# Kernel tuning notes

Hardware: AMD Instinct MI355X
Metric: run time of the kernel (lower is better)

Reference implementation:

```python
import jax, jax.numpy as jnp
import numpy as np

N = 16777216  # length of the returns series


def setup_inputs() -> dict:
    key = jax.random.key(0)
    returns = 0.01 * jax.random.normal(key, (N,), dtype=jnp.float32)
    return {
        "returns": returns,
        "omega": jnp.float32(0.01),
        "alpha": jnp.float32(0.1),
        "beta": jnp.float32(0.85),
    }


def reference(returns, omega, alpha, beta):
    # GARCH(1,1): h[0] = var(returns) (unbiased, matching torch.var default);
    # h[t] = omega + alpha * r[t-1]^2 + beta * h[t-1]
    h0 = jnp.var(returns, ddof=1)
    # drivers b_t = omega + alpha * r_{t-1}^2 for t = 1..n-1
    b = omega + alpha * jnp.square(returns[:-1])

    def step(h_prev, b_t):
        h_t = b_t + beta * h_prev
        return h_t, h_t

    _, h_rest = jax.lax.scan(step, h0, b)
    h = jnp.concatenate([h0[None], h_rest])  # [n]
    return jnp.sqrt(h), h
```

## Files before the change

### kernel.cpp

```cpp
#include <hip/hip_runtime.h>
#include <math.h>


#define KPW 2048
#define MAIN_BLOCK 256
#define FIXN 160

__global__ __launch_bounds__(MAIN_BLOCK, 8)
void garch_main(const float* __restrict__ r, int n,
                const float* __restrict__ pOmega, const float* __restrict__ pAlpha,
                const float* __restrict__ pBeta,
                double* __restrict__ partial,
                float* __restrict__ out_sqrt, float* __restrict__ out_h) {
    const int lane = threadIdx.x & 63;
    const int wid  = threadIdx.x >> 6;
    const int gwave = blockIdx.x * (MAIN_BLOCK >> 6) + wid;
    const int start = gwave * KPW;

    const float omega = *pOmega;
    const float alpha = *pAlpha;
    const float beta  = *pBeta;

    double s_acc = 0.0, q_acc = 0.0;

    if (start < n) {
        const float c1 = beta;
        const float c2 = c1 * c1;
        const float c3 = c2 * c1;
        const float c4 = c2 * c2;
        const float c8 = c4 * c4;
        const float c16 = c8 * c8;
        const float c32 = c16 * c16;
        const float c64 = c32 * c32;

        float pw1 = 1.0f;
        {
            float p = beta; int e = lane;
            if (e & 1)  pw1 *= p; p *= p;
            if (e & 2)  pw1 *= p; p *= p;
            if (e & 4)  pw1 *= p; p *= p;
            if (e & 8)  pw1 *= p; p *= p;
            if (e & 16) pw1 *= p; p *= p;
            if (e & 32) pw1 *= p;
        }
        float pw4 = 1.0f;
        {
            float p = c4; int e = lane;
            if (e & 1)  pw4 *= p; p *= p;
            if (e & 2)  pw4 *= p; p *= p;
            if (e & 4)  pw4 *= p; p *= p;
            if (e & 8)  pw4 *= p; p *= p;
            if (e & 16) pw4 *= p; p *= p;
            if (e & 32) pw4 *= p;
        }

        float h_prev, r_carry;
        if (start == 0) {
            h_prev = 0.0f;
            r_carry = 0.0f;
        } else {
            float ra = r[start - 2 - lane];
            float ba = fmaf(alpha * ra, ra, omega);
            float part = pw1 * ba;
            for (int d = 1; d < 64; d <<= 1) part += __shfl_xor(part, d, 64);
            h_prev = part;
            r_carry = r[start - 1];
        }

        int end = start + KPW; if (end > n) end = n;
        const float4* r4p = (const float4*)r;
        const int idx0 = (start >> 2) + lane;
        const int iters = (end - start) >> 8;

        float4 rv;
        if (iters > 0) rv = r4p[idx0];
        for (int it = 0; it < iters; ++it) {
            float4 nx;
            if (it + 1 < iters) nx = r4p[idx0 + ((it + 1) << 6)];

            float sp = (rv.x + rv.y) + (rv.z + rv.w);
            float qp = (rv.x * rv.x + rv.y * rv.y)
                     + (rv.z * rv.z + rv.w * rv.w);
            s_acc += (double)sp;
            q_acc += (double)qp;

            float prev = __shfl_up(rv.w, 1, 64);
            if (lane == 0) prev = r_carry;

            float b0 = fmaf(alpha * prev, prev, omega);
            float b1 = fmaf(alpha * rv.x, rv.x, omega);
            float b2 = fmaf(alpha * rv.y, rv.y, omega);
            float b3 = fmaf(alpha * rv.z, rv.z, omega);

            float B = fmaf(c1, b2, b3);
            B = fmaf(c2, b1, B);
            B = fmaf(c3, b0, B);

            float t;
            t = __shfl_up(B, 1, 64);  if (lane >= 1)  B = fmaf(c4,  t, B);
            t = __shfl_up(B, 2, 64);  if (lane >= 2)  B = fmaf(c8,  t, B);
            t = __shfl_up(B, 4, 64);  if (lane >= 4)  B = fmaf(c16, t, B);
            t = __shfl_up(B, 8, 64);  if (lane >= 8)  B = fmaf(c32, t, B);
            t = __shfl_up(B, 16, 64); if (lane >= 16) B = fmaf(c64, t, B);

            float Bex = __shfl_up(B, 1, 64);
            if (lane == 0) Bex = 0.0f;
            float h_base = fmaf(pw4, h_prev, Bex);

            float h0v = fmaf(c1, h_base, b0);
            float h1v = fmaf(c1, h0v, b1);
            float h2v = fmaf(c1, h1v, b2);
            float h3v = fmaf(c1, h2v, b3);

            const int s = start + (it << 8);
            int idx4 = (s >> 2) + lane;
            reinterpret_cast<float4*>(out_sqrt)[idx4] =
                make_float4(sqrtf(h0v), sqrtf(h1v), sqrtf(h2v), sqrtf(h3v));
            reinterpret_cast<float4*>(out_h)[idx4] =
                make_float4(h0v, h1v, h2v, h3v);

            h_prev  = __shfl(h3v, 63, 64);
            r_carry = __shfl(rv.w, 63, 64);
            rv = nx;
        }

        int s = start + (iters << 8);
        if (s < end && lane == 0) {
            float h = h_prev;
            for (int tt = s; tt < end; ++tt) {
                float rr = (tt > 0) ? r[tt - 1] : 0.0f;
                double dv = (double)rr;
                s_acc += dv; q_acc += dv * dv;
                float b = fmaf(alpha * rr, rr, omega);
                float hv = fmaf(beta, h, b);
                out_sqrt[tt] = sqrtf(hv);
                out_h[tt] = hv;
                h = hv;
            }
        }
    }

    for (int d = 1; d < 64; d <<= 1) {
        s_acc += __shfl_xor(s_acc, d, 64);
        q_acc += __shfl_xor(q_acc, d, 64);
    }
    __shared__ double ls[MAIN_BLOCK / 64], lq[MAIN_BLOCK / 64];
    if (lane == 0) { ls[wid] = s_acc; lq[wid] = q_acc; }
    __syncthreads();
    if (threadIdx.x == 0) {
        double S = 0.0, Q = 0.0;
        for (int w = 0; w < MAIN_BLOCK / 64; ++w) { S += ls[w]; Q += lq[w]; }
        partial[2 * blockIdx.x]     = S;
        partial[2 * blockIdx.x + 1] = Q;
    }
}

__global__ __launch_bounds__(256)
void garch_fixup(const float* __restrict__ r, int n,
                 const double* __restrict__ partial, int nparts,
                 const float* __restrict__ pOmega, const float* __restrict__ pAlpha,
                 const float* __restrict__ pBeta,
                 float* __restrict__ out_sqrt, float* __restrict__ out_h) {
    double s = 0.0, q = 0.0;
    for (int i = threadIdx.x; i < nparts; i += blockDim.x) {
        s += partial[2 * i];
        q += partial[2 * i + 1];
    }
    for (int d = 1; d < 64; d <<= 1) {
        s += __shfl_xor(s, d, 64);
        q += __shfl_xor(q, d, 64);
    }
    __shared__ double ls[4], lq[4];
    int wid = threadIdx.x >> 6, lane = threadIdx.x & 63;
    if (lane == 0) { ls[wid] = s; lq[wid] = q; }

    __shared__ float rs[FIXN];
    int m = (FIXN < n) ? FIXN : n;
    if (threadIdx.x < m) rs[threadIdx.x] = r[threadIdx.x];
    __syncthreads();

    if (threadIdx.x == 0) {
        double S = 0.0, Q = 0.0;
        for (int w = 0; w < 4; ++w) { S += ls[w]; Q += lq[w]; }
        double mean = S / (double)n;
        double var = (Q - (double)n * mean * mean) / (double)(n - 1);
        const float omega = *pOmega;
        const float alpha = *pAlpha;
        const float beta  = *pBeta;
        float h = (float)var;
        out_h[0] = h;
        out_sqrt[0] = sqrtf(h);
        for (int t = 1; t < m; ++t) {
            float rr = rs[t - 1];
            float b = fmaf(alpha * rr, rr, omega);
            h = fmaf(beta, h, b);
            out_h[t] = h;
            out_sqrt[t] = sqrtf(h);
        }
    }
}

extern "C" void kernel_launch(void* const* d_in, const int* in_sizes, int n_in,
                              void* d_out, int out_size, void* d_ws, size_t ws_size,
                              hipStream_t stream) {
    const float* r      = (const float*)d_in[0];
    const float* pOmega = (const float*)d_in[1];
    const float* pAlpha = (const float*)d_in[2];
    const float* pBeta  = (const float*)d_in[3];
    int n = in_sizes[0];

    float* out_sqrt = (float*)d_out;
    float* out_h    = out_sqrt + n;

    double* partial = (double*)d_ws;

    const int elems_per_block = KPW * (MAIN_BLOCK / 64);
    const int nblocks = (n + elems_per_block - 1) / elems_per_block;

    garch_main<<<nblocks, MAIN_BLOCK, 0, stream>>>(
        r, n, pOmega, pAlpha, pBeta, partial, out_sqrt, out_h);
    garch_fixup<<<1, 256, 0, stream>>>(
        r, n, partial, nblocks, pOmega, pAlpha, pBeta, out_sqrt, out_h);
}
```

Measured before the change: 202.7 us.

## Restructure scan to 16 elements per lane via LDS transpose

Each wave now handles batches of 1024 elements. Coalesced float4 loads are transposed through padded LDS so each lane holds 16 consecutive returns and runs a serial 16-step local recurrence. This shrinks the cross-lane shuffle scan from five steps to two per batch, and results are transposed back through LDS for coalesced stores. It trades shuffle latency for LDS traffic and more registers, and launch bounds drop occupancy from 8 to 4 blocks.

```diff
diff --git a/kernel.cpp b/kernel.cpp
--- a/kernel.cpp
+++ b/kernel.cpp
@@ -2,20 +2,25 @@
 #include <math.h>
 
 
-#define KPW 2048
+#define K 16
+#define ROWLEN 20
+#define BATCH 1024
+#define NB 2
 #define MAIN_BLOCK 256
+#define WPB (MAIN_BLOCK/64)
 #define FIXN 160
 
-__global__ __launch_bounds__(MAIN_BLOCK, 8)
+__global__ __launch_bounds__(MAIN_BLOCK, 4)
 void garch_main(const float* __restrict__ r, int n,
                 const float* __restrict__ pOmega, const float* __restrict__ pAlpha,
                 const float* __restrict__ pBeta,
                 double* __restrict__ partial,
                 float* __restrict__ out_sqrt, float* __restrict__ out_h) {
+    __shared__ float lds[WPB][64 * ROWLEN];
     const int lane = threadIdx.x & 63;
     const int wid  = threadIdx.x >> 6;
-    const int gwave = blockIdx.x * (MAIN_BLOCK >> 6) + wid;
-    const int start = gwave * KPW;
+    const int gwave = blockIdx.x * WPB + wid;
+    const int wstart = gwave * (BATCH * NB);
 
     const float omega = *pOmega;
     const float alpha = *pAlpha;
@@ -23,10 +28,8 @@
 
     double s_acc = 0.0, q_acc = 0.0;
 
-    if (start < n) {
-        const float c1 = beta;
-        const float c2 = c1 * c1;
-        const float c3 = c2 * c1;
+    if (wstart < n) {
+        const float c2 = beta * beta;
         const float c4 = c2 * c2;
         const float c8 = c4 * c4;
         const float c16 = c8 * c8;
@@ -43,99 +46,102 @@
             if (e & 16) pw1 *= p; p *= p;
             if (e & 32) pw1 *= p;
         }
-        float pw4 = 1.0f;
-        {
-            float p = c4; int e = lane;
-            if (e & 1)  pw4 *= p; p *= p;
-            if (e & 2)  pw4 *= p; p *= p;
-            if (e & 4)  pw4 *= p; p *= p;
-            if (e & 8)  pw4 *= p; p *= p;
-            if (e & 16) pw4 *= p; p *= p;
-            if (e & 32) pw4 *= p;
-        }
-
-        float h_prev, r_carry;
-        if (start == 0) {
-            h_prev = 0.0f;
-            r_carry = 0.0f;
-        } else {
-            float ra = r[start - 2 - lane];
+        float pw16l;
+        { float a2 = pw1 * pw1; float a4 = a2 * a2; float a8 = a4 * a4; pw16l = a8 * a8; }
+
+        float Wp = 0.0f, rm1 = 0.0f;
+        if (wstart > 0) {
+            float ra = r[wstart - 2 - lane];
             float ba = fmaf(alpha * ra, ra, omega);
             float part = pw1 * ba;
             for (int d = 1; d < 64; d <<= 1) part += __shfl_xor(part, d, 64);
-            h_prev = part;
-            r_carry = r[start - 1];
-        }
-
-        int end = start + KPW; if (end > n) end = n;
+            Wp = part;
+            rm1 = r[wstart - 1];
+        }
+
+        float* buf = &lds[wid][0];
         const float4* r4p = (const float4*)r;
-        const int idx0 = (start >> 2) + lane;
-        const int iters = (end - start) >> 8;
-
-        float4 rv;
-        if (iters > 0) rv = r4p[idx0];
-        for (int it = 0; it < iters; ++it) {
-            float4 nx;
-            if (it + 1 < iters) nx = r4p[idx0 + ((it + 1) << 6)];
-
-            float sp = (rv.x + rv.y) + (rv.z + rv.w);
-            float qp = (rv.x * rv.x + rv.y * rv.y)
-                     + (rv.z * rv.z + rv.w * rv.w);
-            s_acc += (double)sp;
-            q_acc += (double)qp;
-
-            float prev = __shfl_up(rv.w, 1, 64);
-            if (lane == 0) prev = r_carry;
-
-            float b0 = fmaf(alpha * prev, prev, omega);
-            float b1 = fmaf(alpha * rv.x, rv.x, omega);
-            float b2 = fmaf(alpha * rv.y, rv.y, omega);
-            float b3 = fmaf(alpha * rv.z, rv.z, omega);
-
-            float B = fmaf(c1, b2, b3);
-            B = fmaf(c2, b1, B);
-            B = fmaf(c3, b0, B);
-
-            float t;
-            t = __shfl_up(B, 1, 64);  if (lane >= 1)  B = fmaf(c4,  t, B);
-            t = __shfl_up(B, 2, 64);  if (lane >= 2)  B = fmaf(c8,  t, B);
-            t = __shfl_up(B, 4, 64);  if (lane >= 4)  B = fmaf(c16, t, B);
-            t = __shfl_up(B, 8, 64);  if (lane >= 8)  B = fmaf(c32, t, B);
-            t = __shfl_up(B, 16, 64); if (lane >= 16) B = fmaf(c64, t, B);
-
-            float Bex = __shfl_up(B, 1, 64);
-            if (lane == 0) Bex = 0.0f;
-            float h_base = fmaf(pw4, h_prev, Bex);
-
-            float h0v = fmaf(c1, h_base, b0);
-            float h1v = fmaf(c1, h0v, b1);
-            float h2v = fmaf(c1, h1v, b2);
-            float h3v = fmaf(c1, h2v, b3);
-
-            const int s = start + (it << 8);
-            int idx4 = (s >> 2) + lane;
-            reinterpret_cast<float4*>(out_sqrt)[idx4] =
-                make_float4(sqrtf(h0v), sqrtf(h1v), sqrtf(h2v), sqrtf(h3v));
-            reinterpret_cast<float4*>(out_h)[idx4] =
-                make_float4(h0v, h1v, h2v, h3v);
-
-            h_prev  = __shfl(h3v, 63, 64);
-            r_carry = __shfl(rv.w, 63, 64);
-            rv = nx;
-        }
-
-        int s = start + (iters << 8);
-        if (s < end && lane == 0) {
-            float h = h_prev;
-            for (int tt = s; tt < end; ++tt) {
-                float rr = (tt > 0) ? r[tt - 1] : 0.0f;
-                double dv = (double)rr;
-                s_acc += dv; q_acc += dv * dv;
-                float b = fmaf(alpha * rr, rr, omega);
-                float hv = fmaf(beta, h, b);
-                out_sqrt[tt] = sqrtf(hv);
-                out_h[tt] = hv;
-                h = hv;
+        float4* oh4 = (float4*)out_h;
+        float4* os4 = (float4*)out_sqrt;
+
+        for (int bi = 0; bi < NB; ++bi) {
+            const int base = wstart + bi * BATCH;
+            if (base >= n) break;
+            if (base + BATCH <= n) {
+                float sp = 0.0f, qp = 0.0f;
+                #pragma unroll
+                for (int j = 0; j < 4; ++j) {
+                    float4 v = r4p[(base >> 2) + (j << 6) + lane];
+                    sp += (v.x + v.y) + (v.z + v.w);
+                    qp += (v.x * v.x + v.y * v.y) + (v.z * v.z + v.w * v.w);
+                    int row = (j << 4) + (lane >> 2);
+                    *(float4*)&buf[row * ROWLEN + 4 * (lane & 3)] = v;
+                }
+                s_acc += (double)sp; q_acc += (double)qp;
+
+                float rl[K];
+                #pragma unroll
+                for (int m = 0; m < 4; ++m) {
+                    float4 v = *(float4*)&buf[lane * ROWLEN + 4 * m];
+                    rl[4*m+0] = v.x; rl[4*m+1] = v.y; rl[4*m+2] = v.z; rl[4*m+3] = v.w;
+                }
+                float pr = __shfl_up(rl[K-1], 1, 64);
+                if (lane == 0) pr = rm1;
+
+                float bl[K];
+                float W = 0.0f;
+                float prv = pr;
+                #pragma unroll
+                for (int k = 0; k < K; ++k) {
+                    float b = fmaf(alpha * prv, prv, omega);
+                    bl[k] = b;
+                    W = fmaf(beta, W, b);
+                    prv = rl[k];
+                }
+
+                float t1 = __shfl_up(W, 1, 64);
+                float Y1 = (lane >= 1) ? fmaf(c16, t1, W) : W;
+                float t2 = __shfl_up(Y1, 2, 64);
+                float Y2 = (lane >= 2) ? fmaf(c32, t2, Y1) : Y1;
+                float sd = __shfl_up(Y2, 1, 64);
+                if (lane == 0) sd = 0.0f;
+                float seed = fmaf(pw16l, Wp, sd);
+
+                float Wtop  = __shfl(Y2, 63, 64);
+                float rlast = __shfl(rl[K-1], 63, 64);
+
+                float h = seed;
+                #pragma unroll
+                for (int m = 0; m < 4; ++m) {
+                    float h0 = fmaf(beta, h,  bl[4*m+0]);
+                    float h1 = fmaf(beta, h0, bl[4*m+1]);
+                    float h2 = fmaf(beta, h1, bl[4*m+2]);
+                    float h3 = fmaf(beta, h2, bl[4*m+3]);
+                    *(float4*)&buf[lane * ROWLEN + 4 * m] = make_float4(h0, h1, h2, h3);
+                    h = h3;
+                }
+
+                #pragma unroll
+                for (int j = 0; j < 4; ++j) {
+                    int row = (j << 4) + (lane >> 2);
+                    float4 hv = *(float4*)&buf[row * ROWLEN + 4 * (lane & 3)];
+                    int idx4 = (base >> 2) + (j << 6) + lane;
+                    oh4[idx4] = hv;
+                    os4[idx4] = make_float4(sqrtf(hv.x), sqrtf(hv.y),
+                                            sqrtf(hv.z), sqrtf(hv.w));
+                }
+
+                Wp  = fmaf(c64, Wp, Wtop);
+                rm1 = rlast;
+            } else if (lane == 0) {
+                float h = Wp;
+                for (int tt = base; tt < n; ++tt) {
+                    float rr = (tt > 0) ? r[tt - 1] : 0.0f;
+                    double dv = (double)rr; s_acc += dv; q_acc += dv * dv;
+                    float b = fmaf(alpha * rr, rr, omega);
+                    h = fmaf(beta, h, b);
+                    out_h[tt] = h; out_sqrt[tt] = sqrtf(h);
+                }
             }
         }
     }
@@ -144,12 +150,12 @@
         s_acc += __shfl_xor(s_acc, d, 64);
         q_acc += __shfl_xor(q_acc, d, 64);
     }
-    __shared__ double ls[MAIN_BLOCK / 64], lq[MAIN_BLOCK / 64];
-    if (lane == 0) { ls[wid] = s_acc; lq[wid] = q_acc; }
+    __shared__ double lsum[WPB], lsq[WPB];
+    if (lane == 0) { lsum[wid] = s_acc; lsq[wid] = q_acc; }
     __syncthreads();
     if (threadIdx.x == 0) {
         double S = 0.0, Q = 0.0;
-        for (int w = 0; w < MAIN_BLOCK / 64; ++w) { S += ls[w]; Q += lq[w]; }
+        for (int w = 0; w < WPB; ++w) { S += lsum[w]; Q += lsq[w]; }
         partial[2 * blockIdx.x]     = S;
         partial[2 * blockIdx.x + 1] = Q;
     }
@@ -214,7 +220,7 @@
 
     double* partial = (double*)d_ws;
 
-    const int elems_per_block = KPW * (MAIN_BLOCK / 64);
+    const int elems_per_block = BATCH * NB * WPB;
     const int nblocks = (n + elems_per_block - 1) / elems_per_block;
 
     garch_main<<<nblocks, MAIN_BLOCK, 0, stream>>>(
```

New measurement: 202.0 us. No clear change (-0.3%).
